# Kernel tuning notes

Hardware: AMD Instinct MI355X
Metric: run time of the kernel (lower is better)

Reference implementation:

```python
import jax, jax.numpy as jnp
import numpy as np

NUMERICAL_STABILIZER = 1e-3


def relu_kernel(data, projection_matrix):
    # data: [B,L,H,D], projection_matrix: [M,D] -> [B,L,H,M]
    ratio = 1.0 / jnp.sqrt(jnp.asarray(projection_matrix.shape[0], dtype=data.dtype))
    data_dash = ratio * jnp.einsum('blhd,md->blhm', data, projection_matrix)
    return jax.nn.relu(data_dash) + NUMERICAL_STABILIZER


def favor_causal(query, key, value, projection_matrix):
    # query/key/value: [B,L,H,D]; projection_matrix: [M,D]
    qp = relu_kernel(query, projection_matrix)  # [B,L,H,M]
    kp = relu_kernel(key, projection_matrix)    # [B,L,H,M]
    # move L to scan axis: [L,B,H,*]
    qs = jnp.transpose(qp, (1, 0, 2, 3))
    ks = jnp.transpose(kp, (1, 0, 2, 3))
    vs = jnp.transpose(value, (1, 0, 2, 3))

    B, H, M = qs.shape[1], qs.shape[2], qs.shape[3]
    D = vs.shape[3]
    kv0 = jnp.zeros((B, H, M, D), dtype=qs.dtype)
    ksum0 = jnp.zeros((B, H, M), dtype=qs.dtype)

    def step(carry, inp):
        kv_sum, k_sum = carry
        q_t, k_t, v_t = inp  # [B,H,M], [B,H,M], [B,H,D]
        kv_sum = kv_sum + jnp.einsum('bhm,bhd->bhmd', k_t, v_t)
        k_sum = k_sum + k_t
        num_t = jnp.einsum('bhmd,bhm->bhd', kv_sum, q_t)  # [B,H,D]
        den_t = jnp.einsum('bhm,bhm->bh', q_t, k_sum)     # [B,H]
        return (kv_sum, k_sum), (num_t, den_t)

    _, (num, den) = jax.lax.scan(step, (kv0, ksum0), (qs, ks, vs))
    # num: [L,B,H,D], den: [L,B,H]
    out = num / den[..., None]
    return jnp.transpose(out, (1, 0, 2, 3))  # [B,L,H,D]


def setup_inputs() -> dict:
    key = jax.random.key(0)
    k1, k2, k3, k4 = jax.random.split(key, 4)
    B, L, H, D, M = 2, 4096, 8, 64, 128
    return {
        'query': jax.random.normal(k1, (B, L, H, D), dtype=jnp.float32),
        'key': jax.random.normal(k2, (B, L, H, D), dtype=jnp.float32),
        'value': jax.random.normal(k3, (B, L, H, D), dtype=jnp.float32),
        'projection_matrix': jax.random.normal(k4, (M, D), dtype=jnp.float32),
    }


def reference(query, key, value, projection_matrix):
    return favor_causal(query, key, value, projection_matrix)
```

## Files before the change

kernel.cpp:

```cpp
#include <hip/hip_runtime.h>


#define B_ 2
#define L_ 4096
#define H_ 8
#define D_ 64
#define M_ 128
#define BH_ 16
#define HD_ 512
#define LHD_ (L_*HD_)
#define C_ 64
#define T_ 64
#define RATIO 0.08838834764831845f
#define EPS 1e-3f

#define REC_CS 8320
#define REC_F  8192
#define CS_TOT (BH_*C_*REC_CS)
#define QF_OFF CS_TOT
#define KF_OFF (CS_TOT + BH_*C_*REC_F)

#define VT_S  72
#define KFT_S 72
#define SM_S  72

typedef __attribute__((ext_vector_type(8))) short bf16x8;
typedef __attribute__((ext_vector_type(4))) short bf16x4;
typedef __attribute__((ext_vector_type(4))) float f32x4;

__device__ __forceinline__ short f2bf(float f) {
  union { float f; unsigned u; } x; x.f = f;
  unsigned r = (x.u + 0x7fffu + ((x.u >> 16) & 1u)) >> 16;
  return (short)r;
}
__device__ __forceinline__ float bf2f(short s) {
  union { unsigned u; float f; } x; x.u = ((unsigned)(unsigned short)s) << 16;
  return x.f;
}
__device__ __forceinline__ bf16x8 load_cvt8(const float* p) {
  float4 a = *(const float4*)p;
  float4 b = *(const float4*)(p + 4);
  union { bf16x8 v; short s[8]; } u;
  u.s[0]=f2bf(a.x); u.s[1]=f2bf(a.y); u.s[2]=f2bf(a.z); u.s[3]=f2bf(a.w);
  u.s[4]=f2bf(b.x); u.s[5]=f2bf(b.y); u.s[6]=f2bf(b.z); u.s[7]=f2bf(b.w);
  return u.v;
}
#define MFMA(a,b,c) __builtin_amdgcn_mfma_f32_16x16x32_bf16((a),(b),(c),0,0,0)

__global__ __launch_bounds__(256) void p1(
    const float* __restrict__ qq, const float* __restrict__ kk,
    const float* __restrict__ vv, const float* __restrict__ P,
    unsigned short* __restrict__ ws)
{
  __shared__ short Vt[64*VT_S];
  __shared__ short Kft[128*KFT_S];

  const int tid = threadIdx.x, bid = blockIdx.x;
  const int bh = bid >> 6, c = bid & 63;
  const int b = bh >> 3, h = bh & 7;
  const int lane = tid & 63, w = tid >> 6, quad = lane >> 4, l15 = lane & 15;
  const size_t gbase = (size_t)b*LHD_ + (size_t)h*D_;
  const int t0 = c*T_;

  for (int fi = tid; fi < 64*16; fi += 256) {
    int t = fi >> 4, d4 = (fi & 15)*4;
    float4 v4 = *(const float4*)(vv + gbase + (size_t)(t0+t)*HD_ + d4);
    Vt[(d4+0)*VT_S + t] = f2bf(v4.x);
    Vt[(d4+1)*VT_S + t] = f2bf(v4.y);
    Vt[(d4+2)*VT_S + t] = f2bf(v4.z);
    Vt[(d4+3)*VT_S + t] = f2bf(v4.w);
  }

  const float* qrow = qq + gbase + (size_t)(t0 + 16*w + l15)*HD_;
  const float* krow = kk + gbase + (size_t)(t0 + 16*w + l15)*HD_;
  bf16x8 aq0 = load_cvt8(qrow + quad*8);
  bf16x8 aq1 = load_cvt8(qrow + 32 + quad*8);
  bf16x8 ak0 = load_cvt8(krow + quad*8);
  bf16x8 ak1 = load_cvt8(krow + 32 + quad*8);
  unsigned short* qfb = ws + QF_OFF + (size_t)(bh*C_+c)*REC_F;
  unsigned short* kfb = ws + KF_OFF + (size_t)(bh*C_+c)*REC_F;
  #pragma unroll
  for (int ct = 0; ct < 8; ++ct) {
    const float* prow = P + (ct*16 + l15)*64;
    bf16x8 bp0 = load_cvt8(prow + quad*8);
    bf16x8 bp1 = load_cvt8(prow + 32 + quad*8);
    f32x4 qa = {0.f,0.f,0.f,0.f}, ka = {0.f,0.f,0.f,0.f};
    qa = MFMA(aq0,bp0,qa); qa = MFMA(aq1,bp1,qa);
    ka = MFMA(ak0,bp0,ka); ka = MFMA(ak1,bp1,ka);
    #pragma unroll
    for (int reg = 0; reg < 4; ++reg) {
      int trow = 16*w + quad*4 + reg;
      int m = l15 + 16*ct;
      short qv = f2bf(fmaxf(qa[reg]*RATIO, 0.f) + EPS);
      short kv = f2bf(fmaxf(ka[reg]*RATIO, 0.f) + EPS);
      qfb[trow*128 + m] = (unsigned short)qv;
      kfb[trow*128 + m] = (unsigned short)kv;
      Kft[m*KFT_S + trow] = kv;
    }
  }
  __syncthreads();

  unsigned short* csb = ws + (size_t)(bh*C_+c)*REC_CS;
  bf16x8 av0 = *(const bf16x8*)&Vt[(16*w + l15)*VT_S + quad*8];
  bf16x8 av1 = *(const bf16x8*)&Vt[(16*w + l15)*VT_S + 32 + quad*8];
  #pragma unroll
  for (int mt = 0; mt < 8; ++mt) {
    f32x4 acc = {0.f,0.f,0.f,0.f};
    bf16x8 b0 = *(const bf16x8*)&Kft[(16*mt + l15)*KFT_S + quad*8];
    bf16x8 b1 = *(const bf16x8*)&Kft[(16*mt + l15)*KFT_S + 32 + quad*8];
    acc = MFMA(av0, b0, acc);
    acc = MFMA(av1, b1, acc);
    #pragma unroll
    for (int reg = 0; reg < 4; ++reg) {
      int d = 16*w + quad*4 + reg;
      int m = l15 + 16*mt;
      csb[d*128 + m] = (unsigned short)f2bf(acc[reg]);
    }
  }
  if (tid < 128) {
    float s = 0.f;
    #pragma unroll 8
    for (int t = 0; t < 64; ++t) s += bf2f(Kft[tid*KFT_S + t]);
    csb[64*128 + tid] = (unsigned short)f2bf(s);
  }
}

__global__ __launch_bounds__(256) void p2(unsigned short* __restrict__ ws)
{
  const int gid = blockIdx.x*256 + threadIdx.x;
  if (gid >= BH_*(REC_CS/4)) return;
  const int bh = gid / (REC_CS/4), g = gid % (REC_CS/4);
  unsigned short* base = ws + (size_t)bh*C_*REC_CS + g*4;
  float run[4] = {0.f,0.f,0.f,0.f};
  #pragma unroll 1
  for (int c = 0; c < C_; c += 4) {
    bf16x4 r[4];
    #pragma unroll
    for (int u = 0; u < 4; ++u)
      r[u] = *(const bf16x4*)(base + (size_t)(c+u)*REC_CS);
    #pragma unroll
    for (int u = 0; u < 4; ++u) {
      union { bf16x4 v; short s[4]; } wv;
      #pragma unroll
      for (int j = 0; j < 4; ++j) { wv.s[j] = f2bf(run[j]); run[j] += bf2f(r[u][j]); }
      *(bf16x4*)(base + (size_t)(c+u)*REC_CS) = wv.v;
    }
  }
}

__global__ __launch_bounds__(256) void p3(
    const float* __restrict__ vv, const unsigned short* __restrict__ ws,
    float* __restrict__ out)
{
  __shared__ short Vt[64*VT_S];
  __shared__ short Sm[64*SM_S];
  __shared__ float ks_lds[128];

  const int tid = threadIdx.x, bid = blockIdx.x;
  const int bh = bid >> 6, c = bid & 63;
  const int b = bh >> 3, h = bh & 7;
  const int lane = tid & 63, w = tid >> 6, quad = lane >> 4, l15 = lane & 15;
  const size_t gbase = (size_t)b*LHD_ + (size_t)h*D_;
  const int t0 = c*T_;
  const unsigned short* csb = ws + (size_t)(bh*C_+c)*REC_CS;
  const unsigned short* qfb = ws + QF_OFF + (size_t)(bh*C_+c)*REC_F;
  const unsigned short* kfb = ws + KF_OFF + (size_t)(bh*C_+c)*REC_F;

  for (int fi = tid; fi < 64*16; fi += 256) {
    int t = fi >> 4, d4 = (fi & 15)*4;
    float4 v4 = *(const float4*)(vv + gbase + (size_t)(t0+t)*HD_ + d4);
    Vt[(d4+0)*VT_S + t] = f2bf(v4.x);
    Vt[(d4+1)*VT_S + t] = f2bf(v4.y);
    Vt[(d4+2)*VT_S + t] = f2bf(v4.z);
    Vt[(d4+3)*VT_S + t] = f2bf(v4.w);
  }
  if (tid < 128) ks_lds[tid] = bf2f((short)csb[64*128 + tid]);

  bf16x8 qf[4];
  #pragma unroll
  for (int ks2 = 0; ks2 < 4; ++ks2)
    qf[ks2] = *(const bf16x8*)(qfb + (16*w + l15)*128 + ks2*32 + quad*8);

  __syncthreads();

  f32x4 nacc[4];
  #pragma unroll
  for (int ct = 0; ct < 4; ++ct) { f32x4 z = {0.f,0.f,0.f,0.f}; nacc[ct] = z; }
  #pragma unroll
  for (int ks2 = 0; ks2 < 4; ++ks2) {
    #pragma unroll
    for (int ct = 0; ct < 4; ++ct) {
      bf16x8 bb = *(const bf16x8*)(csb + (16*ct + l15)*128 + ks2*32 + quad*8);
      nacc[ct] = MFMA(qf[ks2], bb, nacc[ct]);
    }
  }

  float dp = 0.f;
  #pragma unroll
  for (int ks2 = 0; ks2 < 4; ++ks2)
    #pragma unroll
    for (int j = 0; j < 8; ++j)
      dp += bf2f(qf[ks2][j]) * ks_lds[ks2*32 + quad*8 + j];
  dp += __shfl_xor(dp, 16);
  dp += __shfl_xor(dp, 32);

  f32x4 sacc[4];
  #pragma unroll
  for (int jt = 0; jt < 4; ++jt) { f32x4 z = {0.f,0.f,0.f,0.f}; sacc[jt] = z; }
  #pragma unroll
  for (int ks2 = 0; ks2 < 4; ++ks2) {
    #pragma unroll
    for (int jt = 0; jt < 4; ++jt) {
      bf16x8 bb = *(const bf16x8*)(kfb + (16*jt + l15)*128 + ks2*32 + quad*8);
      sacc[jt] = MFMA(qf[ks2], bb, sacc[jt]);
    }
  }
  float rs[4] = {0.f,0.f,0.f,0.f};
  #pragma unroll
  for (int jt = 0; jt < 4; ++jt)
    #pragma unroll
    for (int reg = 0; reg < 4; ++reg) {
      int row = 16*w + quad*4 + reg;
      int j = l15 + 16*jt;
      float val = (j <= row) ? sacc[jt][reg] : 0.f;
      rs[reg] += val;
      Sm[row*SM_S + j] = f2bf(val);
    }
  #pragma unroll
  for (int reg = 0; reg < 4; ++reg) {
    rs[reg] += __shfl_xor(rs[reg], 1);
    rs[reg] += __shfl_xor(rs[reg], 2);
    rs[reg] += __shfl_xor(rs[reg], 4);
    rs[reg] += __shfl_xor(rs[reg], 8);
  }

  #pragma unroll
  for (int ks = 0; ks < 2; ++ks) {
    bf16x8 a = *(const bf16x8*)&Sm[(16*w + l15)*SM_S + ks*32 + quad*8];
    #pragma unroll
    for (int ct = 0; ct < 4; ++ct) {
      bf16x8 bb = *(const bf16x8*)&Vt[(16*ct + l15)*VT_S + ks*32 + quad*8];
      nacc[ct] = MFMA(a, bb, nacc[ct]);
    }
  }

  #pragma unroll
  for (int reg = 0; reg < 4; ++reg) {
    float den1 = __shfl(dp, 4*quad + reg);
    float inv = 1.f / (den1 + rs[reg]);
    int trow = t0 + 16*w + quad*4 + reg;
    #pragma unroll
    for (int ct = 0; ct < 4; ++ct)
      out[gbase + (size_t)trow*HD_ + 16*ct + l15] = nacc[ct][reg] * inv;
  }
}

extern "C" void kernel_launch(void* const* d_in, const int* in_sizes, int n_in,
                              void* d_out, int out_size, void* d_ws, size_t ws_size,
                              hipStream_t stream) {
  const float* q = (const float*)d_in[0];
  const float* k = (const float*)d_in[1];
  const float* v = (const float*)d_in[2];
  const float* P = (const float*)d_in[3];
  float* out = (float*)d_out;
  unsigned short* ws = (unsigned short*)d_ws;

  dim3 blk(256);
  p1<<<dim3(BH_*C_), blk, 0, stream>>>(q, k, v, P, ws);
  p2<<<dim3((BH_*(REC_CS/4) + 255)/256), blk, 0, stream>>>(ws);
  p3<<<dim3(BH_*C_), blk, 0, stream>>>(v, ws, out);
}
```

Baseline: 146.3 us.

## Fuse three phases into one cooperative kernel with grid syncs and LDS-resident features

Replaces the three-launch pipeline with a single cooperative kernel. Each block handles two chunks, keeps the query and key features and the V tile in LDS or registers across a grid-wide sync, and runs the chunk prefix scan in between. This drops the global round-trip of the q/k feature maps and two kernel launches. The cost is two grid syncs, larger LDS use per block, and a prefix scan parallelised over fewer elements per thread. A fallback to three kernels is kept if the cooperative launch fails; that path recomputes features in the last phase instead of reloading them.

```diff
diff --git a/kernel.cpp b/kernel.cpp
--- a/kernel.cpp
+++ b/kernel.cpp
@@ -1,4 +1,7 @@
 #include <hip/hip_runtime.h>
+#include <hip/hip_cooperative_groups.h>
+
+namespace cg = cooperative_groups;
 
 
 #define B_ 2
@@ -13,19 +16,13 @@
 #define T_ 64
 #define RATIO 0.08838834764831845f
 #define EPS 1e-3f
-
 #define REC_CS 8320
-#define REC_F  8192
-#define CS_TOT (BH_*C_*REC_CS)
-#define QF_OFF CS_TOT
-#define KF_OFF (CS_TOT + BH_*C_*REC_F)
-
-#define VT_S  72
-#define KFT_S 72
-#define SM_S  72
+
+#define VT_S 72
+#define KF_S 136
+#define SCR_SZ 9216
 
 typedef __attribute__((ext_vector_type(8))) short bf16x8;
-typedef __attribute__((ext_vector_type(4))) short bf16x4;
 typedef __attribute__((ext_vector_type(4))) float f32x4;
 
 __device__ __forceinline__ short f2bf(float f) {
@@ -47,21 +44,8 @@
 }
 #define MFMA(a,b,c) __builtin_amdgcn_mfma_f32_16x16x32_bf16((a),(b),(c),0,0,0)
 
-__global__ __launch_bounds__(256) void p1(
-    const float* __restrict__ qq, const float* __restrict__ kk,
-    const float* __restrict__ vv, const float* __restrict__ P,
-    unsigned short* __restrict__ ws)
-{
-  __shared__ short Vt[64*VT_S];
-  __shared__ short Kft[128*KFT_S];
-
-  const int tid = threadIdx.x, bid = blockIdx.x;
-  const int bh = bid >> 6, c = bid & 63;
-  const int b = bh >> 3, h = bh & 7;
-  const int lane = tid & 63, w = tid >> 6, quad = lane >> 4, l15 = lane & 15;
-  const size_t gbase = (size_t)b*LHD_ + (size_t)h*D_;
-  const int t0 = c*T_;
-
+__device__ __forceinline__ void stageVt(short* Vt, const float* __restrict__ vv,
+                                        size_t gbase, int t0, int tid) {
   for (int fi = tid; fi < 64*16; fi += 256) {
     int t = fi >> 4, d4 = (fi & 15)*4;
     float4 v4 = *(const float4*)(vv + gbase + (size_t)(t0+t)*HD_ + d4);
@@ -70,15 +54,20 @@
     Vt[(d4+2)*VT_S + t] = f2bf(v4.z);
     Vt[(d4+3)*VT_S + t] = f2bf(v4.w);
   }
-
+}
+
+__device__ __forceinline__ void features(
+    const float* __restrict__ qq, const float* __restrict__ kk,
+    const float* __restrict__ P, short* __restrict__ Kf_lds,
+    short* __restrict__ Scr, int w, int quad, int l15,
+    size_t gbase, int t0, bf16x8 qfr[4], f32x4 kasave[8])
+{
   const float* qrow = qq + gbase + (size_t)(t0 + 16*w + l15)*HD_;
   const float* krow = kk + gbase + (size_t)(t0 + 16*w + l15)*HD_;
   bf16x8 aq0 = load_cvt8(qrow + quad*8);
   bf16x8 aq1 = load_cvt8(qrow + 32 + quad*8);
   bf16x8 ak0 = load_cvt8(krow + quad*8);
   bf16x8 ak1 = load_cvt8(krow + 32 + quad*8);
-  unsigned short* qfb = ws + QF_OFF + (size_t)(bh*C_+c)*REC_F;
-  unsigned short* kfb = ws + KF_OFF + (size_t)(bh*C_+c)*REC_F;
   #pragma unroll
   for (int ct = 0; ct < 8; ++ct) {
     const float* prow = P + (ct*16 + l15)*64;
@@ -87,120 +76,97 @@
     f32x4 qa = {0.f,0.f,0.f,0.f}, ka = {0.f,0.f,0.f,0.f};
     qa = MFMA(aq0,bp0,qa); qa = MFMA(aq1,bp1,qa);
     ka = MFMA(ak0,bp0,ka); ka = MFMA(ak1,bp1,ka);
+    kasave[ct] = ka;
     #pragma unroll
     for (int reg = 0; reg < 4; ++reg) {
-      int trow = 16*w + quad*4 + reg;
-      int m = l15 + 16*ct;
-      short qv = f2bf(fmaxf(qa[reg]*RATIO, 0.f) + EPS);
-      short kv = f2bf(fmaxf(ka[reg]*RATIO, 0.f) + EPS);
-      qfb[trow*128 + m] = (unsigned short)qv;
-      kfb[trow*128 + m] = (unsigned short)kv;
-      Kft[m*KFT_S + trow] = kv;
-    }
-  }
-  __syncthreads();
-
-  unsigned short* csb = ws + (size_t)(bh*C_+c)*REC_CS;
-  bf16x8 av0 = *(const bf16x8*)&Vt[(16*w + l15)*VT_S + quad*8];
-  bf16x8 av1 = *(const bf16x8*)&Vt[(16*w + l15)*VT_S + 32 + quad*8];
-  #pragma unroll
-  for (int mt = 0; mt < 8; ++mt) {
-    f32x4 acc = {0.f,0.f,0.f,0.f};
-    bf16x8 b0 = *(const bf16x8*)&Kft[(16*mt + l15)*KFT_S + quad*8];
-    bf16x8 b1 = *(const bf16x8*)&Kft[(16*mt + l15)*KFT_S + 32 + quad*8];
-    acc = MFMA(av0, b0, acc);
-    acc = MFMA(av1, b1, acc);
-    #pragma unroll
-    for (int reg = 0; reg < 4; ++reg) {
-      int d = 16*w + quad*4 + reg;
-      int m = l15 + 16*mt;
-      csb[d*128 + m] = (unsigned short)f2bf(acc[reg]);
-    }
-  }
+      int trow = 16*w + 4*quad + reg;
+      int m = 16*ct + l15;
+      Scr   [trow*KF_S + m] = f2bf(fmaxf(qa[reg]*RATIO, 0.f) + EPS);
+      Kf_lds[trow*KF_S + m] = f2bf(fmaxf(ka[reg]*RATIO, 0.f) + EPS);
+    }
+  }
+  #pragma unroll
+  for (int k2 = 0; k2 < 4; ++k2)
+    qfr[k2] = *(const bf16x8*)&Scr[(16*w + l15)*KF_S + k2*32 + quad*8];
+}
+
+__device__ __forceinline__ void writeKft(short* Scr, const f32x4 kasave[8],
+                                         int w, int quad, int l15) {
+  #pragma unroll
+  for (int ct = 0; ct < 8; ++ct)
+    #pragma unroll
+    for (int reg = 0; reg < 4; ++reg)
+      Scr[(16*ct + l15)*VT_S + 16*w + 4*quad + reg] =
+          f2bf(fmaxf(kasave[ct][reg]*RATIO, 0.f) + EPS);
+}
+
+__device__ __forceinline__ void chunkSums(const short* Scr , const short* Vt,
+    unsigned short* __restrict__ csb, int tid, int w, int quad, int l15)
+{
   if (tid < 128) {
     float s = 0.f;
     #pragma unroll 8
-    for (int t = 0; t < 64; ++t) s += bf2f(Kft[tid*KFT_S + t]);
-    csb[64*128 + tid] = (unsigned short)f2bf(s);
-  }
-}
-
-__global__ __launch_bounds__(256) void p2(unsigned short* __restrict__ ws)
-{
-  const int gid = blockIdx.x*256 + threadIdx.x;
-  if (gid >= BH_*(REC_CS/4)) return;
-  const int bh = gid / (REC_CS/4), g = gid % (REC_CS/4);
-  unsigned short* base = ws + (size_t)bh*C_*REC_CS + g*4;
-  float run[4] = {0.f,0.f,0.f,0.f};
-  #pragma unroll 1
+    for (int t = 0; t < 64; ++t) s += bf2f(Scr[tid*VT_S + t]);
+    csb[8192 + tid] = (unsigned short)f2bf(s);
+  }
+  bf16x8 av0 = *(const bf16x8*)&Vt[(16*w + l15)*VT_S + quad*8];
+  bf16x8 av1 = *(const bf16x8*)&Vt[(16*w + l15)*VT_S + 32 + quad*8];
+  #pragma unroll
+  for (int mt = 0; mt < 8; ++mt) {
+    f32x4 acc = {0.f,0.f,0.f,0.f};
+    bf16x8 b0 = *(const bf16x8*)&Scr[(16*mt + l15)*VT_S + quad*8];
+    bf16x8 b1 = *(const bf16x8*)&Scr[(16*mt + l15)*VT_S + 32 + quad*8];
+    acc = MFMA(av0, b0, acc);
+    acc = MFMA(av1, b1, acc);
+    #pragma unroll
+    for (int reg = 0; reg < 4; ++reg)
+      csb[(16*w + 4*quad + reg)*128 + 16*mt + l15] = (unsigned short)f2bf(acc[reg]);
+  }
+}
+
+__device__ __forceinline__ void prefixB(unsigned short* __restrict__ ws, int gid) {
+  if (gid >= BH_*(REC_CS/2)) return;
+  int bh = gid / (REC_CS/2), rem = gid % (REC_CS/2);
+  unsigned short* base = ws + (size_t)bh*C_*REC_CS + (size_t)rem*2;
+  float r0 = 0.f, r1 = 0.f;
   for (int c = 0; c < C_; c += 4) {
-    bf16x4 r[4];
-    #pragma unroll
-    for (int u = 0; u < 4; ++u)
-      r[u] = *(const bf16x4*)(base + (size_t)(c+u)*REC_CS);
-    #pragma unroll
-    for (int u = 0; u < 4; ++u) {
-      union { bf16x4 v; short s[4]; } wv;
-      #pragma unroll
-      for (int j = 0; j < 4; ++j) { wv.s[j] = f2bf(run[j]); run[j] += bf2f(r[u][j]); }
-      *(bf16x4*)(base + (size_t)(c+u)*REC_CS) = wv.v;
-    }
-  }
-}
-
-__global__ __launch_bounds__(256) void p3(
-    const float* __restrict__ vv, const unsigned short* __restrict__ ws,
-    float* __restrict__ out)
-{
-  __shared__ short Vt[64*VT_S];
-  __shared__ short Sm[64*SM_S];
-  __shared__ float ks_lds[128];
-
-  const int tid = threadIdx.x, bid = blockIdx.x;
-  const int bh = bid >> 6, c = bid & 63;
-  const int b = bh >> 3, h = bh & 7;
-  const int lane = tid & 63, w = tid >> 6, quad = lane >> 4, l15 = lane & 15;
-  const size_t gbase = (size_t)b*LHD_ + (size_t)h*D_;
-  const int t0 = c*T_;
-  const unsigned short* csb = ws + (size_t)(bh*C_+c)*REC_CS;
-  const unsigned short* qfb = ws + QF_OFF + (size_t)(bh*C_+c)*REC_F;
-  const unsigned short* kfb = ws + KF_OFF + (size_t)(bh*C_+c)*REC_F;
-
-  for (int fi = tid; fi < 64*16; fi += 256) {
-    int t = fi >> 4, d4 = (fi & 15)*4;
-    float4 v4 = *(const float4*)(vv + gbase + (size_t)(t0+t)*HD_ + d4);
-    Vt[(d4+0)*VT_S + t] = f2bf(v4.x);
-    Vt[(d4+1)*VT_S + t] = f2bf(v4.y);
-    Vt[(d4+2)*VT_S + t] = f2bf(v4.z);
-    Vt[(d4+3)*VT_S + t] = f2bf(v4.w);
-  }
-  if (tid < 128) ks_lds[tid] = bf2f((short)csb[64*128 + tid]);
-
-  bf16x8 qf[4];
-  #pragma unroll
-  for (int ks2 = 0; ks2 < 4; ++ks2)
-    qf[ks2] = *(const bf16x8*)(qfb + (16*w + l15)*128 + ks2*32 + quad*8);
-
-  __syncthreads();
-
+    unsigned u[4];
+    #pragma unroll
+    for (int j = 0; j < 4; ++j)
+      u[j] = *(const unsigned*)(base + (size_t)(c+j)*REC_CS);
+    #pragma unroll
+    for (int j = 0; j < 4; ++j) {
+      unsigned pw = (unsigned)(unsigned short)f2bf(r0)
+                  | ((unsigned)(unsigned short)f2bf(r1) << 16);
+      *(unsigned*)(base + (size_t)(c+j)*REC_CS) = pw;
+      r0 += bf2f((short)(u[j] & 0xffffu));
+      r1 += bf2f((short)(u[j] >> 16));
+    }
+  }
+}
+
+__device__ __forceinline__ void phaseCcore(
+    const unsigned short* __restrict__ csb, const short* Kf_lds, const short* Vt,
+    short* Scr , const float* ksl, const bf16x8 qfr[4],
+    float* __restrict__ out, size_t gbase, int t0, int w, int quad, int l15)
+{
   f32x4 nacc[4];
   #pragma unroll
   for (int ct = 0; ct < 4; ++ct) { f32x4 z = {0.f,0.f,0.f,0.f}; nacc[ct] = z; }
   #pragma unroll
-  for (int ks2 = 0; ks2 < 4; ++ks2) {
+  for (int k2 = 0; k2 < 4; ++k2)
     #pragma unroll
     for (int ct = 0; ct < 4; ++ct) {
-      bf16x8 bb = *(const bf16x8*)(csb + (16*ct + l15)*128 + ks2*32 + quad*8);
-      nacc[ct] = MFMA(qf[ks2], bb, nacc[ct]);
-    }
-  }
+      bf16x8 bb = *(const bf16x8*)(csb + (16*ct + l15)*128 + k2*32 + quad*8);
+      nacc[ct] = MFMA(qfr[k2], bb, nacc[ct]);
+    }
 
   float dp = 0.f;
   #pragma unroll
-  for (int ks2 = 0; ks2 < 4; ++ks2)
+  for (int k2 = 0; k2 < 4; ++k2)
     #pragma unroll
     for (int j = 0; j < 8; ++j)
-      dp += bf2f(qf[ks2][j]) * ks_lds[ks2*32 + quad*8 + j];
+      dp += bf2f(qfr[k2][j]) * ksl[k2*32 + quad*8 + j];
   dp += __shfl_xor(dp, 16);
   dp += __shfl_xor(dp, 32);
 
@@ -208,23 +174,22 @@
   #pragma unroll
   for (int jt = 0; jt < 4; ++jt) { f32x4 z = {0.f,0.f,0.f,0.f}; sacc[jt] = z; }
   #pragma unroll
-  for (int ks2 = 0; ks2 < 4; ++ks2) {
+  for (int k2 = 0; k2 < 4; ++k2)
     #pragma unroll
     for (int jt = 0; jt < 4; ++jt) {
-      bf16x8 bb = *(const bf16x8*)(kfb + (16*jt + l15)*128 + ks2*32 + quad*8);
-      sacc[jt] = MFMA(qf[ks2], bb, sacc[jt]);
-    }
-  }
+      bf16x8 bb = *(const bf16x8*)&Kf_lds[(16*jt + l15)*KF_S + k2*32 + quad*8];
+      sacc[jt] = MFMA(qfr[k2], bb, sacc[jt]);
+    }
   float rs[4] = {0.f,0.f,0.f,0.f};
   #pragma unroll
   for (int jt = 0; jt < 4; ++jt)
     #pragma unroll
     for (int reg = 0; reg < 4; ++reg) {
-      int row = 16*w + quad*4 + reg;
-      int j = l15 + 16*jt;
+      int row = 16*w + 4*quad + reg;
+      int j = 16*jt + l15;
       float val = (j <= row) ? sacc[jt][reg] : 0.f;
       rs[reg] += val;
-      Sm[row*SM_S + j] = f2bf(val);
+      Scr[row*VT_S + j] = f2bf(val);
     }
   #pragma unroll
   for (int reg = 0; reg < 4; ++reg) {
@@ -233,26 +198,124 @@
     rs[reg] += __shfl_xor(rs[reg], 4);
     rs[reg] += __shfl_xor(rs[reg], 8);
   }
-
-  #pragma unroll
-  for (int ks = 0; ks < 2; ++ks) {
-    bf16x8 a = *(const bf16x8*)&Sm[(16*w + l15)*SM_S + ks*32 + quad*8];
+  #pragma unroll
+  for (int kx = 0; kx < 2; ++kx) {
+    bf16x8 a = *(const bf16x8*)&Scr[(16*w + l15)*VT_S + kx*32 + quad*8];
     #pragma unroll
     for (int ct = 0; ct < 4; ++ct) {
-      bf16x8 bb = *(const bf16x8*)&Vt[(16*ct + l15)*VT_S + ks*32 + quad*8];
+      bf16x8 bb = *(const bf16x8*)&Vt[(16*ct + l15)*VT_S + kx*32 + quad*8];
       nacc[ct] = MFMA(a, bb, nacc[ct]);
     }
   }
-
   #pragma unroll
   for (int reg = 0; reg < 4; ++reg) {
     float den1 = __shfl(dp, 4*quad + reg);
     float inv = 1.f / (den1 + rs[reg]);
-    int trow = t0 + 16*w + quad*4 + reg;
+    int trow = t0 + 16*w + 4*quad + reg;
     #pragma unroll
     for (int ct = 0; ct < 4; ++ct)
       out[gbase + (size_t)trow*HD_ + 16*ct + l15] = nacc[ct][reg] * inv;
   }
+}
+
+__global__ __launch_bounds__(256, 2) void fused_coop(
+    const float* __restrict__ qq, const float* __restrict__ kk,
+    const float* __restrict__ vv, const float* __restrict__ P,
+    unsigned short* __restrict__ ws, float* __restrict__ out)
+{
+  __shared__ alignas(16) short Vt[2][64*VT_S];
+  __shared__ alignas(16) short Kf[2][64*KF_S];
+  __shared__ alignas(16) short Scr[SCR_SZ];
+  __shared__ float ksl[2][128];
+
+  cg::grid_group grid = cg::this_grid();
+  const int tid = threadIdx.x, w = tid >> 6, quad = (tid >> 4) & 3, l15 = tid & 15;
+  const int cid0 = blockIdx.x * 2;
+  bf16x8 qfr[2][4];
+
+  #pragma unroll
+  for (int s = 0; s < 2; ++s) {
+    const int cid = cid0 + s, bh = cid >> 6, c = cid & 63;
+    const size_t gbase = (size_t)(bh >> 3)*LHD_ + (size_t)(bh & 7)*D_;
+    const int t0 = c*T_;
+    unsigned short* csb = ws + (size_t)cid*REC_CS;
+
+    stageVt(Vt[s], vv, gbase, t0, tid);
+    f32x4 kasave[8];
+    features(qq, kk, P, Kf[s], Scr, w, quad, l15, gbase, t0, qfr[s], kasave);
+    __syncthreads();
+    writeKft(Scr, kasave, w, quad, l15);
+    __syncthreads();
+    chunkSums(Scr, Vt[s], csb, tid, w, quad, l15);
+    __syncthreads();
+  }
+
+  grid.sync();
+  prefixB(ws, blockIdx.x*256 + tid);
+  grid.sync();
+
+  {
+    int s2 = tid >> 7, m = tid & 127;
+    const unsigned short* csbS = ws + (size_t)(cid0 + s2)*REC_CS;
+    ksl[s2][m] = bf2f((short)csbS[8192 + m]);
+  }
+  __syncthreads();
+  #pragma unroll
+  for (int s = 0; s < 2; ++s) {
+    const int cid = cid0 + s, bh = cid >> 6, c = cid & 63;
+    const size_t gbase = (size_t)(bh >> 3)*LHD_ + (size_t)(bh & 7)*D_;
+    const int t0 = c*T_;
+    const unsigned short* csb = ws + (size_t)cid*REC_CS;
+    phaseCcore(csb, Kf[s], Vt[s], Scr, ksl[s], qfr[s], out, gbase, t0, w, quad, l15);
+  }
+}
+
+__global__ __launch_bounds__(256, 2) void pA(
+    const float* __restrict__ qq, const float* __restrict__ kk,
+    const float* __restrict__ vv, const float* __restrict__ P,
+    unsigned short* __restrict__ ws)
+{
+  __shared__ alignas(16) short Vt[64*VT_S];
+  __shared__ alignas(16) short Kf1[64*KF_S];
+  __shared__ alignas(16) short Scr[SCR_SZ];
+  const int tid = threadIdx.x, w = tid >> 6, quad = (tid >> 4) & 3, l15 = tid & 15;
+  const int cid = blockIdx.x, bh = cid >> 6, c = cid & 63;
+  const size_t gbase = (size_t)(bh >> 3)*LHD_ + (size_t)(bh & 7)*D_;
+  const int t0 = c*T_;
+  unsigned short* csb = ws + (size_t)cid*REC_CS;
+  stageVt(Vt, vv, gbase, t0, tid);
+  bf16x8 qfr[4]; f32x4 kasave[8];
+  features(qq, kk, P, Kf1, Scr, w, quad, l15, gbase, t0, qfr, kasave);
+  __syncthreads();
+  writeKft(Scr, kasave, w, quad, l15);
+  __syncthreads();
+  chunkSums(Scr, Vt, csb, tid, w, quad, l15);
+}
+
+__global__ __launch_bounds__(256) void pB(unsigned short* __restrict__ ws) {
+  prefixB(ws, blockIdx.x*256 + threadIdx.x);
+}
+
+__global__ __launch_bounds__(256, 2) void pC(
+    const float* __restrict__ qq, const float* __restrict__ kk,
+    const float* __restrict__ vv, const float* __restrict__ P,
+    unsigned short* __restrict__ ws, float* __restrict__ out)
+{
+  __shared__ alignas(16) short Vt[64*VT_S];
+  __shared__ alignas(16) short Kf1[64*KF_S];
+  __shared__ alignas(16) short Scr[SCR_SZ];
+  __shared__ float ksl[128];
+  const int tid = threadIdx.x, w = tid >> 6, quad = (tid >> 4) & 3, l15 = tid & 15;
+  const int cid = blockIdx.x, bh = cid >> 6, c = cid & 63;
+  const size_t gbase = (size_t)(bh >> 3)*LHD_ + (size_t)(bh & 7)*D_;
+  const int t0 = c*T_;
+  const unsigned short* csb = ws + (size_t)cid*REC_CS;
+  stageVt(Vt, vv, gbase, t0, tid);
+  bf16x8 qfr[4]; f32x4 kasave[8];
+  features(qq, kk, P, Kf1, Scr, w, quad, l15, gbase, t0, qfr, kasave);
+  if (tid < 128) ksl[tid] = bf2f((short)csb[8192 + tid]);
+  __syncthreads();
+  phaseCcore(csb, Kf1, Vt, Scr, ksl, qfr, out, gbase, t0, w, quad, l15);
 }
 
 extern "C" void kernel_launch(void* const* d_in, const int* in_sizes, int n_in,
@@ -265,8 +328,12 @@
   float* out = (float*)d_out;
   unsigned short* ws = (unsigned short*)d_ws;
 
-  dim3 blk(256);
-  p1<<<dim3(BH_*C_), blk, 0, stream>>>(q, k, v, P, ws);
-  p2<<<dim3((BH_*(REC_CS/4) + 255)/256), blk, 0, stream>>>(ws);
-  p3<<<dim3(BH_*C_), blk, 0, stream>>>(v, ws, out);
-}
+  void* args[] = {(void*)&q, (void*)&k, (void*)&v, (void*)&P, (void*)&ws, (void*)&out};
+  hipError_t e = hipLaunchCooperativeKernel((const void*)fused_coop,
+                                            dim3(BH_*C_/2), dim3(256), args, 0, stream);
+  if (e != hipSuccess) {
+    pA<<<dim3(BH_*C_), dim3(256), 0, stream>>>(q, k, v, P, ws);
+    pB<<<dim3((BH_*(REC_CS/2) + 255)/256), dim3(256), 0, stream>>>(ws);
+    pC<<<dim3(BH_*C_), dim3(256), 0, stream>>>(q, k, v, P, ws, out);
+  }
+}
```

After: 268.2 us. 1.83x slower.
